# Performance work log

Measured on AMD Instinct MI355X. Metric: run time of the kernel, lower is better.

## Reference

```python
import jax, jax.numpy as jnp
import numpy as np

N_NODES = 50000


def _degree_norm(src, dst, n):
    # symmetric GCN normalization with self-loops already appended
    deg = jax.ops.segment_sum(jnp.ones(src.shape[0], jnp.float32), dst, num_segments=n)
    dinv = jnp.where(deg > 0, jax.lax.rsqrt(deg), 0.0)
    return dinv[src] * dinv[dst]  # [E_full]


def _gcn_layer(x, W, b, src, dst, norm, n):
    h = x @ W                                  # [N, out]
    msgs = h[src] * norm[:, None]              # gather + scale, [E_full, out]
    out = jax.ops.segment_sum(msgs, dst, num_segments=n)
    return out + b


def setup_inputs() -> dict:
    key = jax.random.key(0)
    k1, k2, k3, k4 = jax.random.split(key, 4)
    n, e, d_in, d_out = N_NODES, 800000, 256, 128
    x = jax.random.normal(k1, (n, d_in), jnp.float32)
    edge_index = jax.random.randint(k2, (2, e), 0, n, dtype=jnp.int64)
    W1 = jax.random.normal(k3, (d_in, 2 * d_out), jnp.float32) / np.sqrt(d_in)
    b1 = jnp.zeros((2 * d_out,), jnp.float32)
    W2 = jax.random.normal(k4, (2 * d_out, d_out), jnp.float32) / np.sqrt(2 * d_out)
    b2 = jnp.zeros((d_out,), jnp.float32)
    return {"x": x, "edge_index": edge_index, "W1": W1, "b1": b1, "W2": W2, "b2": b2}


def reference(x, edge_index, W1, b1, W2, b2):
    n = x.shape[0]
    loops = jnp.arange(n, dtype=edge_index.dtype)
    src = jnp.concatenate([edge_index[0], loops])
    dst = jnp.concatenate([edge_index[1], loops])
    norm = _degree_norm(src, dst, n)
    h = jax.nn.relu(_gcn_layer(x, W1, b1, src, dst, norm, n))
    h = jax.nn.relu(_gcn_layer(h, W2, b2, src, dst, norm, n))
    return h
```

## Files before the change

### kernel.cpp

```cpp
#include <hip/hip_runtime.h>
#include <hip/hip_bf16.h>


typedef __attribute__((ext_vector_type(8))) short bf16x8;
typedef __attribute__((ext_vector_type(8))) unsigned short u16x8;
typedef __attribute__((ext_vector_type(4))) float f32x4;

__device__ inline float bf2f(unsigned short u) {
    return __uint_as_float(((unsigned)u) << 16);
}
__device__ inline unsigned short f2bf(float f) {
    unsigned x = __float_as_uint(f);
    unsigned r = (x + 0x7fffu + ((x >> 16) & 1u)) >> 16;
    return (unsigned short)r;
}

__global__ void degree_kernel(const int* __restrict__ dst, unsigned* __restrict__ deg, int E) {
    int e = blockIdx.x * blockDim.x + threadIdx.x;
    if (e < E) atomicAdd(&deg[dst[e]], 1u);
}

__global__ void dinv_kernel(const unsigned* __restrict__ deg, float* __restrict__ dinv, int N) {
    int i = blockIdx.x * blockDim.x + threadIdx.x;
    if (i < N) dinv[i] = rsqrtf((float)(deg[i] + 1u));
}

#define NBIN 512

__global__ __launch_bounds__(256) void hist_lds_kernel(const unsigned* __restrict__ deg,
                                                       int* __restrict__ hist, int N) {
    __shared__ int lh[NBIN];
    const int t = threadIdx.x;
#pragma unroll
    for (int i = 0; i < NBIN / 256; i++) lh[t + i * 256] = 0;
    __syncthreads();
    int idx = blockIdx.x * 256 + t;
    if (idx < N) {
        int b = (int)deg[idx]; if (b > NBIN - 1) b = NBIN - 1;
        atomicAdd(&lh[NBIN - 1 - b], 1);
    }
    __syncthreads();
#pragma unroll
    for (int i = 0; i < NBIN / 256; i++) {
        int v = lh[t + i * 256];
        if (v) atomicAdd(&hist[t + i * 256], v);
    }
}

__global__ __launch_bounds__(256) void place_lds_kernel(const unsigned* __restrict__ deg,
                                                        int* __restrict__ hist,
                                                        int* __restrict__ perm, int N) {
    __shared__ int lh[NBIN];
    __shared__ int base[NBIN];
    const int t = threadIdx.x;
#pragma unroll
    for (int i = 0; i < NBIN / 256; i++) lh[t + i * 256] = 0;
    __syncthreads();
    int idx = blockIdx.x * 256 + t;
    int bin = 0, rank = 0;
    if (idx < N) {
        int b = (int)deg[idx]; if (b > NBIN - 1) b = NBIN - 1;
        bin = NBIN - 1 - b;
        rank = atomicAdd(&lh[bin], 1);
    }
    __syncthreads();
#pragma unroll
    for (int i = 0; i < NBIN / 256; i++) {
        int v = lh[t + i * 256];
        if (v) base[t + i * 256] = atomicAdd(&hist[t + i * 256], v);
    }
    __syncthreads();
    if (idx < N) perm[base[bin] + rank] = idx;
}

__global__ __launch_bounds__(256) void rank_kernel(const int* __restrict__ perm,
                                                   int* __restrict__ rank, int N) {
    int i = blockIdx.x * blockDim.x + threadIdx.x;
    if (i < N) rank[perm[i]] = i;
}

#define SCAN_CHUNK 2048

__global__ __launch_bounds__(256) void scan_phase1(const unsigned* __restrict__ deg,
                                                   const int* __restrict__ perm,
                                                   int* __restrict__ bsum, int N) {
    __shared__ int ws[4];
    const int t = threadIdx.x, lane = t & 63, w = t >> 6;
    int base = blockIdx.x * SCAN_CHUNK;
    int s = 0;
#pragma unroll
    for (int r = 0; r < SCAN_CHUNK / 256; r++) {
        int i = base + r * 256 + t;
        s += (i < N) ? (int)deg[perm[i]] : 0;
    }
#pragma unroll
    for (int off = 1; off < 64; off <<= 1) s += __shfl_xor(s, off, 64);
    if (lane == 0) ws[w] = s;
    __syncthreads();
    if (t == 0) bsum[blockIdx.x] = ws[0] + ws[1] + ws[2] + ws[3];
}

__global__ void scan_phase2(int* __restrict__ bsum, int nb) {
    const int t = threadIdx.x;
    int carry = 0;
    for (int b = 0; b < nb; b += 64) {
        int i = b + t;
        int v = (i < nb) ? bsum[i] : 0;
        int x = v;
#pragma unroll
        for (int off = 1; off < 64; off <<= 1) {
            int y = __shfl_up(x, off, 64);
            if (t >= off) x += y;
        }
        if (i < nb) bsum[i] = carry + x - v;
        carry += __shfl(x, 63, 64);
    }
}

__global__ __launch_bounds__(256) void scan_phase3(const unsigned* __restrict__ deg,
                                                   const int* __restrict__ perm,
                                                   const int* __restrict__ bsum,
                                                   int* __restrict__ rowptr,
                                                   int* __restrict__ cursor, int N) {
    __shared__ int ws[4];
    const int t = threadIdx.x, lane = t & 63, w = t >> 6;
    int base = blockIdx.x * SCAN_CHUNK;
    int carry = bsum[blockIdx.x];
#pragma unroll
    for (int r = 0; r < SCAN_CHUNK / 256; r++) {
        int i = base + r * 256 + t;
        int v = (i < N) ? (int)deg[perm[i]] : 0;
        int x = v;
#pragma unroll
        for (int off = 1; off < 64; off <<= 1) {
            int y = __shfl_up(x, off, 64);
            if (lane >= off) x += y;
        }
        if (lane == 63) ws[w] = x;
        __syncthreads();
        int wo = 0;
        for (int j = 0; j < w; j++) wo += ws[j];
        int excl = x + wo - v;
        if (i < N) { rowptr[i] = carry + excl; cursor[i] = carry + excl; }
        int total = ws[0] + ws[1] + ws[2] + ws[3];
        __syncthreads();
        carry += total;
    }
    if (blockIdx.x == gridDim.x - 1 && t == 0) rowptr[N] = carry;
}

__global__ __launch_bounds__(256) void fill_kernel(const int* __restrict__ src,
                                                   const int* __restrict__ dst,
                                                   const int* __restrict__ rank,
                                                   int* __restrict__ cursor,
                                                   unsigned short* __restrict__ col, int E) {
    int e = blockIdx.x * blockDim.x + threadIdx.x;
    if (e < E) {
        int d = dst[e];
        int pos = atomicAdd(&cursor[rank[d]], 1);
        col[pos] = (unsigned short)src[e];
    }
}

__global__ __launch_bounds__(256) void convert_x_kernel(const float* __restrict__ in,
                                                        const float* __restrict__ dinv,
                                                        unsigned short* __restrict__ out,
                                                        long n4, int ld4) {
    long i = (long)blockIdx.x * blockDim.x + threadIdx.x;
    if (i < n4) {
        float ds = dinv[i / ld4];
        float4 v = ((const float4*)in)[i];
        ushort4 o;
        o.x = f2bf(v.x * ds); o.y = f2bf(v.y * ds);
        o.z = f2bf(v.z * ds); o.w = f2bf(v.w * ds);
        ((ushort4*)out)[i] = o;
    }
}

__global__ __launch_bounds__(256) void convert_wt_kernel(const float* __restrict__ W,
                                                         unsigned short* __restrict__ WT,
                                                         int K, int Nw) {
    int id = blockIdx.x * blockDim.x + threadIdx.x;
    if (id < K * Nw) {
        int k = id / Nw;
        int n = id % Nw;
        WT[(long)n * K + k] = f2bf(W[id]);
    }
}

#define GBM 128
#define GBN 128
#define GBK 64
template <int CH>
__global__ __launch_bounds__(256) void gemm_bf16(const unsigned short* __restrict__ A,
                                                 const unsigned short* __restrict__ BT,
                                                 unsigned short* __restrict__ C,
                                                 int M, int Nc, int K) {
    __shared__ __align__(16) unsigned short As[GBM * GBK];
    __shared__ __align__(16) unsigned short Bs[GBN * GBK];
    const int t = threadIdx.x;
    const int lane = t & 63;
    const int w = t >> 6;
    const int row0 = blockIdx.x * GBM;
    const int col0 = blockIdx.y * GBN;
    const int rb = (w >> 1) * 64;
    const int cb = (w & 1) * 64;

    f32x4 acc[4][4] = {};

    for (int kb = 0; kb < K; kb += GBK) {
#pragma unroll
        for (int i = 0; i < 4; i++) {
            int p = i * 256 + t;
            int row = p >> 3;
            int slot = p & 7;
            int chunk = slot ^ (row & 7);
            int grow = row0 + row;
            if (grow >= M) grow = M - 1;
            const unsigned short* src = A + (size_t)grow * K + kb + chunk * 8;
            __builtin_amdgcn_global_load_lds(
                (const __attribute__((address_space(1))) void*)src,
                (__attribute__((address_space(3))) void*)&As[p * 8], 16, 0, 0);
        }
#pragma unroll
        for (int i = 0; i < 4; i++) {
            int p = i * 256 + t;
            int row = p >> 3;
            int slot = p & 7;
            int chunk = slot ^ (row & 7);
            const unsigned short* src = BT + (size_t)(col0 + row) * K + kb + chunk * 8;
            __builtin_amdgcn_global_load_lds(
                (const __attribute__((address_space(1))) void*)src,
                (__attribute__((address_space(3))) void*)&Bs[p * 8], 16, 0, 0);
        }
        asm volatile("s_waitcnt vmcnt(0)" ::: "memory");
        __syncthreads();

#pragma unroll
        for (int ks = 0; ks < 2; ks++) {
            int kq = ks * 4 + (lane >> 4);
            int rsel = lane & 15;
            bf16x8 af[4], bfr[4];
#pragma unroll
            for (int mt = 0; mt < 4; mt++) {
                int m = rb + mt * 16 + rsel;
                int slot = kq ^ (m & 7);
                af[mt] = *(const bf16x8*)&As[m * GBK + slot * 8];
            }
#pragma unroll
            for (int nt = 0; nt < 4; nt++) {
                int n = cb + nt * 16 + rsel;
                int slot = kq ^ (n & 7);
                bfr[nt] = *(const bf16x8*)&Bs[n * GBK + slot * 8];
            }
#pragma unroll
            for (int mt = 0; mt < 4; mt++)
#pragma unroll
                for (int nt = 0; nt < 4; nt++)
                    acc[mt][nt] = __builtin_amdgcn_mfma_f32_16x16x32_bf16(
                        af[mt], bfr[nt], acc[mt][nt], 0, 0, 0);
        }
        __syncthreads();
    }

#pragma unroll
    for (int mt = 0; mt < 4; mt++) {
#pragma unroll
        for (int nt = 0; nt < 4; nt++) {
            int gcol = col0 + cb + nt * 16 + (lane & 15);
            int c = gcol / CH;
            int fo = gcol % CH;
            int grow0 = row0 + rb + mt * 16 + 4 * (lane >> 4);
#pragma unroll
            for (int r = 0; r < 4; r++) {
                int g = grow0 + r;
                if (g < M)
                    C[((size_t)c * M + g) * CH + fo] = f2bf(acc[mt][nt][r]);
            }
        }
    }
}

template <int CH, int NCH, bool OUT_BF16>
__global__ __launch_bounds__(256) void gather_cm_kernel(
    const unsigned short* __restrict__ h_cm,
    const int* __restrict__ rowptr,
    const unsigned short* __restrict__ col,
    const int* __restrict__ perm,
    const float* __restrict__ dinv,
    const float* __restrict__ bias,
    void* __restrict__ out,
    int Nn, int F) {
    constexpr int LF = CH / 8;
    constexpr int NS = 64 / LF;
    constexpr int NPB = NS * 4;
    const int chunk = blockIdx.x % NCH;
    const int g = blockIdx.x / NCH;
    const int w = threadIdx.x >> 6;
    const int lane = threadIdx.x & 63;
    const int fl = lane & (LF - 1);
    const int ns = lane / LF;
    const int idx = g * NPB + w * NS + ns;
    const bool valid = idx < Nn;
    const int cidx = valid ? idx : Nn - 1;
    const int node = perm[cidx];

    const unsigned short* hc = h_cm + (size_t)chunk * Nn * CH;
    const int beg = rowptr[cidx];
    const int end = valid ? rowptr[cidx + 1] : beg;
    const float ddst = dinv[node];
    const int fo = fl * 8;

    float a[8] = {};
    int e = beg;
    for (; e + 4 <= end; e += 4) {
        int s0 = col[e], s1 = col[e + 1], s2 = col[e + 2], s3 = col[e + 3];
        u16x8 u0 = *(const u16x8*)(hc + s0 * CH + fo);
        u16x8 u1 = *(const u16x8*)(hc + s1 * CH + fo);
        u16x8 u2 = *(const u16x8*)(hc + s2 * CH + fo);
        u16x8 u3 = *(const u16x8*)(hc + s3 * CH + fo);
#pragma unroll
        for (int j = 0; j < 8; j++) {
            a[j] += (bf2f(u0[j]) + bf2f(u1[j])) + (bf2f(u2[j]) + bf2f(u3[j]));
        }
    }
    for (; e < end; e++) {
        int s = col[e];
        u16x8 u = *(const u16x8*)(hc + s * CH + fo);
#pragma unroll
        for (int j = 0; j < 8; j++) a[j] += bf2f(u[j]);
    }

    if (valid) {
        u16x8 us = *(const u16x8*)(hc + node * CH + fo);
        const int f0g = chunk * CH + fo;
        f32x4 bv0 = *(const f32x4*)(bias + f0g);
        f32x4 bv1 = *(const f32x4*)(bias + f0g + 4);
        float v[8];
#pragma unroll
        for (int j = 0; j < 8; j++) {
            float b = (j < 4) ? bv0[j] : bv1[j - 4];
            v[j] = fmaxf(fmaf(a[j] + bf2f(us[j]), ddst, b), 0.f);
        }
        if (OUT_BF16) {
            u16x8 o;
#pragma unroll
            for (int j = 0; j < 8; j++) o[j] = f2bf(v[j] * ddst);
            *(u16x8*)((unsigned short*)out + (size_t)node * F + f0g) = o;
        } else {
            f32x4 o0, o1;
#pragma unroll
            for (int j = 0; j < 4; j++) { o0[j] = v[j]; o1[j] = v[j + 4]; }
            float* op = (float*)out + (size_t)node * F + f0g;
            *(f32x4*)op = o0;
            *(f32x4*)(op + 4) = o1;
        }
    }
}

extern "C" void kernel_launch(void* const* d_in, const int* in_sizes, int n_in,
                              void* d_out, int out_size, void* d_ws, size_t ws_size,
                              hipStream_t stream) {
    const float* x  = (const float*)d_in[0];
    const int* ei   = (const int*)d_in[1];
    const float* W1 = (const float*)d_in[2];
    const float* b1 = (const float*)d_in[3];
    const float* W2 = (const float*)d_in[4];
    const float* b2 = (const float*)d_in[5];

    const int DIN = 256;
    const int N = in_sizes[0] / DIN;
    const int E = in_sizes[1] / 2;
    const int H = in_sizes[3];
    const int DOUT = in_sizes[5];

    const int* src = ei;
    const int* dst = ei + E;

    char* ws = (char*)d_ws;
    unsigned* deg = (unsigned*)ws;                   ws += (size_t)N * 4;
    float* dinv   = (float*)ws;                      ws += (size_t)N * 4;
    int* rowptr   = (int*)ws;                        ws += (size_t)(N + 4) * 4;
    int* bsum     = (int*)ws;                        ws += 64 * 4;
    int* hist     = (int*)ws;                        ws += NBIN * 4;
    int* perm     = (int*)ws;                        ws += (size_t)N * 4;
    int* rankv    = (int*)ws;                        ws += (size_t)N * 4;
    int* cursor   = (int*)ws;                        ws += (size_t)N * 4;
    unsigned short* col = (unsigned short*)ws;       ws += (size_t)E * 2;
    unsigned short* xb  = (unsigned short*)ws;       ws += (size_t)N * DIN * 2;
    unsigned short* w1t = (unsigned short*)ws;       ws += (size_t)DIN * H * 2;
    unsigned short* w2t = (unsigned short*)ws;       ws += (size_t)H * DOUT * 2;
    unsigned short* h1b = (unsigned short*)ws;       ws += (size_t)N * H * 2;
    unsigned short* y1b = (unsigned short*)ws;       ws += (size_t)N * H * 2;
    unsigned short* h2b = xb;
    float* outp = (float*)d_out;

    hipMemsetAsync(deg, 0, (size_t)N * 4, stream);
    hipMemsetAsync(hist, 0, (size_t)NBIN * 4, stream);
    degree_kernel<<<(E + 255) / 256, 256, 0, stream>>>(dst, deg, E);
    dinv_kernel<<<(N + 255) / 256, 256, 0, stream>>>(deg, dinv, N);
    hist_lds_kernel<<<(N + 255) / 256, 256, 0, stream>>>(deg, hist, N);
    scan_phase2<<<1, 64, 0, stream>>>(hist, NBIN);
    place_lds_kernel<<<(N + 255) / 256, 256, 0, stream>>>(deg, hist, perm, N);
    rank_kernel<<<(N + 255) / 256, 256, 0, stream>>>(perm, rankv, N);
    {
        int nb = (N + SCAN_CHUNK - 1) / SCAN_CHUNK;
        scan_phase1<<<nb, 256, 0, stream>>>(deg, perm, bsum, N);
        scan_phase2<<<1, 64, 0, stream>>>(bsum, nb);
        scan_phase3<<<nb, 256, 0, stream>>>(deg, perm, bsum, rowptr, cursor, N);
    }
    fill_kernel<<<(E + 255) / 256, 256, 0, stream>>>(src, dst, rankv, cursor, col, E);

    {
        long n4 = (long)N * DIN / 4;
        convert_x_kernel<<<(int)((n4 + 255) / 256), 256, 0, stream>>>(x, dinv, xb, n4, DIN / 4);
        convert_wt_kernel<<<(DIN * H + 255) / 256, 256, 0, stream>>>(W1, w1t, DIN, H);
        convert_wt_kernel<<<(H * DOUT + 255) / 256, 256, 0, stream>>>(W2, w2t, H, DOUT);
    }

    {
        dim3 grid((N + GBM - 1) / GBM, H / GBN);
        gemm_bf16<32><<<grid, 256, 0, stream>>>(xb, w1t, h1b, N, H, DIN);
    }
    {
        constexpr int NPB1 = (64 / (32 / 8)) * 4;
        gather_cm_kernel<32, 8, true><<<8 * ((N + NPB1 - 1) / NPB1), 256, 0, stream>>>(
            h1b, rowptr, col, perm, dinv, b1, y1b, N, H);
    }

    {
        dim3 grid((N + GBM - 1) / GBM, DOUT / GBN);
        gemm_bf16<32><<<grid, 256, 0, stream>>>(y1b, w2t, h2b, N, DOUT, H);
    }
    {
        constexpr int NPB2 = (64 / (32 / 8)) * 4;
        gather_cm_kernel<32, 4, false><<<4 * ((N + NPB2 - 1) / NPB2), 256, 0, stream>>>(
            h2b, rowptr, col, perm, dinv, b2, outp, N, DOUT);
    }
}
```

Before: 356.7 us.

## Derive CSR row pointers from degree-bin offsets and unroll gather by eight

```diff
diff --git a/kernel.cpp b/kernel.cpp
--- a/kernel.cpp
+++ b/kernel.cpp
@@ -47,9 +47,41 @@
     }
 }
 
-__global__ __launch_bounds__(256) void place_lds_kernel(const unsigned* __restrict__ deg,
-                                                        int* __restrict__ hist,
-                                                        int* __restrict__ perm, int N) {
+__global__ void scan_bins_kernel(const int* __restrict__ hist,
+                                 int* __restrict__ binstart,
+                                 int* __restrict__ bincur,
+                                 int* __restrict__ edgebase,
+                                 int* __restrict__ rowptr, int N, int E) {
+    const int t = threadIdx.x;
+    int cn = 0, ce = 0;
+    for (int b = 0; b < NBIN; b += 64) {
+        int i = b + t;
+        int cnt = hist[i];
+        int d = NBIN - 1 - i;
+        int en = cnt * d;
+        int xn = cnt, xe = en;
+#pragma unroll
+        for (int off = 1; off < 64; off <<= 1) {
+            int yn = __shfl_up(xn, off, 64);
+            int ye = __shfl_up(xe, off, 64);
+            if (t >= off) { xn += yn; xe += ye; }
+        }
+        binstart[i] = cn + xn - cnt;
+        bincur[i]   = cn + xn - cnt;
+        edgebase[i] = ce + xe - en;
+        cn += __shfl(xn, 63, 64);
+        ce += __shfl(xe, 63, 64);
+    }
+    if (t == 0) rowptr[N] = E;
+}
+
+__global__ __launch_bounds__(256) void place_fused_kernel(
+    const unsigned* __restrict__ deg,
+    int* __restrict__ bincur,
+    const int* __restrict__ binstart,
+    const int* __restrict__ edgebase,
+    int* __restrict__ perm, int* __restrict__ rankv,
+    int* __restrict__ rowptr, int* __restrict__ cursor, int N) {
     __shared__ int lh[NBIN];
     __shared__ int base[NBIN];
     const int t = threadIdx.x;
@@ -57,96 +89,28 @@
     for (int i = 0; i < NBIN / 256; i++) lh[t + i * 256] = 0;
     __syncthreads();
     int idx = blockIdx.x * 256 + t;
-    int bin = 0, rank = 0;
+    int bin = 0, lrank = 0;
     if (idx < N) {
         int b = (int)deg[idx]; if (b > NBIN - 1) b = NBIN - 1;
         bin = NBIN - 1 - b;
-        rank = atomicAdd(&lh[bin], 1);
+        lrank = atomicAdd(&lh[bin], 1);
     }
     __syncthreads();
 #pragma unroll
     for (int i = 0; i < NBIN / 256; i++) {
         int v = lh[t + i * 256];
-        if (v) base[t + i * 256] = atomicAdd(&hist[t + i * 256], v);
+        if (v) base[t + i * 256] = atomicAdd(&bincur[t + i * 256], v);
     }
     __syncthreads();
-    if (idx < N) perm[base[bin] + rank] = idx;
-}
-
-__global__ __launch_bounds__(256) void rank_kernel(const int* __restrict__ perm,
-                                                   int* __restrict__ rank, int N) {
-    int i = blockIdx.x * blockDim.x + threadIdx.x;
-    if (i < N) rank[perm[i]] = i;
-}
-
-#define SCAN_CHUNK 2048
-
-__global__ __launch_bounds__(256) void scan_phase1(const unsigned* __restrict__ deg,
-                                                   const int* __restrict__ perm,
-                                                   int* __restrict__ bsum, int N) {
-    __shared__ int ws[4];
-    const int t = threadIdx.x, lane = t & 63, w = t >> 6;
-    int base = blockIdx.x * SCAN_CHUNK;
-    int s = 0;
-#pragma unroll
-    for (int r = 0; r < SCAN_CHUNK / 256; r++) {
-        int i = base + r * 256 + t;
-        s += (i < N) ? (int)deg[perm[i]] : 0;
-    }
-#pragma unroll
-    for (int off = 1; off < 64; off <<= 1) s += __shfl_xor(s, off, 64);
-    if (lane == 0) ws[w] = s;
-    __syncthreads();
-    if (t == 0) bsum[blockIdx.x] = ws[0] + ws[1] + ws[2] + ws[3];
-}
-
-__global__ void scan_phase2(int* __restrict__ bsum, int nb) {
-    const int t = threadIdx.x;
-    int carry = 0;
-    for (int b = 0; b < nb; b += 64) {
-        int i = b + t;
-        int v = (i < nb) ? bsum[i] : 0;
-        int x = v;
-#pragma unroll
-        for (int off = 1; off < 64; off <<= 1) {
-            int y = __shfl_up(x, off, 64);
-            if (t >= off) x += y;
-        }
-        if (i < nb) bsum[i] = carry + x - v;
-        carry += __shfl(x, 63, 64);
-    }
-}
-
-__global__ __launch_bounds__(256) void scan_phase3(const unsigned* __restrict__ deg,
-                                                   const int* __restrict__ perm,
-                                                   const int* __restrict__ bsum,
-                                                   int* __restrict__ rowptr,
-                                                   int* __restrict__ cursor, int N) {
-    __shared__ int ws[4];
-    const int t = threadIdx.x, lane = t & 63, w = t >> 6;
-    int base = blockIdx.x * SCAN_CHUNK;
-    int carry = bsum[blockIdx.x];
-#pragma unroll
-    for (int r = 0; r < SCAN_CHUNK / 256; r++) {
-        int i = base + r * 256 + t;
-        int v = (i < N) ? (int)deg[perm[i]] : 0;
-        int x = v;
-#pragma unroll
-        for (int off = 1; off < 64; off <<= 1) {
-            int y = __shfl_up(x, off, 64);
-            if (lane >= off) x += y;
-        }
-        if (lane == 63) ws[w] = x;
-        __syncthreads();
-        int wo = 0;
-        for (int j = 0; j < w; j++) wo += ws[j];
-        int excl = x + wo - v;
-        if (i < N) { rowptr[i] = carry + excl; cursor[i] = carry + excl; }
-        int total = ws[0] + ws[1] + ws[2] + ws[3];
-        __syncthreads();
-        carry += total;
-    }
-    if (blockIdx.x == gridDim.x - 1 && t == 0) rowptr[N] = carry;
+    if (idx < N) {
+        int pos = base[bin] + lrank;
+        int d = NBIN - 1 - bin;
+        int rp = edgebase[bin] + (pos - binstart[bin]) * d;
+        perm[pos] = idx;
+        rankv[idx] = pos;
+        rowptr[pos] = rp;
+        cursor[pos] = rp;
+    }
 }
 
 __global__ __launch_bounds__(256) void fill_kernel(const int* __restrict__ src,
@@ -311,8 +275,25 @@
     const float ddst = dinv[node];
     const int fo = fl * 8;
 
-    float a[8] = {};
+    float a0[8] = {}, a1[8] = {};
     int e = beg;
+    for (; e + 8 <= end; e += 8) {
+        int s0 = col[e],     s1 = col[e + 1], s2 = col[e + 2], s3 = col[e + 3];
+        int s4 = col[e + 4], s5 = col[e + 5], s6 = col[e + 6], s7 = col[e + 7];
+        u16x8 u0 = *(const u16x8*)(hc + s0 * CH + fo);
+        u16x8 u1 = *(const u16x8*)(hc + s1 * CH + fo);
+        u16x8 u2 = *(const u16x8*)(hc + s2 * CH + fo);
+        u16x8 u3 = *(const u16x8*)(hc + s3 * CH + fo);
+        u16x8 u4 = *(const u16x8*)(hc + s4 * CH + fo);
+        u16x8 u5 = *(const u16x8*)(hc + s5 * CH + fo);
+        u16x8 u6 = *(const u16x8*)(hc + s6 * CH + fo);
+        u16x8 u7 = *(const u16x8*)(hc + s7 * CH + fo);
+#pragma unroll
+        for (int j = 0; j < 8; j++) {
+            a0[j] += (bf2f(u0[j]) + bf2f(u1[j])) + (bf2f(u2[j]) + bf2f(u3[j]));
+            a1[j] += (bf2f(u4[j]) + bf2f(u5[j])) + (bf2f(u6[j]) + bf2f(u7[j]));
+        }
+    }
     for (; e + 4 <= end; e += 4) {
         int s0 = col[e], s1 = col[e + 1], s2 = col[e + 2], s3 = col[e + 3];
         u16x8 u0 = *(const u16x8*)(hc + s0 * CH + fo);
@@ -321,14 +302,14 @@
         u16x8 u3 = *(const u16x8*)(hc + s3 * CH + fo);
 #pragma unroll
         for (int j = 0; j < 8; j++) {
-            a[j] += (bf2f(u0[j]) + bf2f(u1[j])) + (bf2f(u2[j]) + bf2f(u3[j]));
+            a0[j] += (bf2f(u0[j]) + bf2f(u1[j])) + (bf2f(u2[j]) + bf2f(u3[j]));
         }
     }
     for (; e < end; e++) {
         int s = col[e];
         u16x8 u = *(const u16x8*)(hc + s * CH + fo);
 #pragma unroll
-        for (int j = 0; j < 8; j++) a[j] += bf2f(u[j]);
+        for (int j = 0; j < 8; j++) a1[j] += bf2f(u[j]);
     }
 
     if (valid) {
@@ -340,7 +321,8 @@
 #pragma unroll
         for (int j = 0; j < 8; j++) {
             float b = (j < 4) ? bv0[j] : bv1[j - 4];
-            v[j] = fmaxf(fmaf(a[j] + bf2f(us[j]), ddst, b), 0.f);
+            float s = (a0[j] + a1[j]) + bf2f(us[j]);
+            v[j] = fmaxf(fmaf(s, ddst, b), 0.f);
         }
         if (OUT_BF16) {
             u16x8 o;
@@ -381,8 +363,10 @@
     unsigned* deg = (unsigned*)ws;                   ws += (size_t)N * 4;
     float* dinv   = (float*)ws;                      ws += (size_t)N * 4;
     int* rowptr   = (int*)ws;                        ws += (size_t)(N + 4) * 4;
-    int* bsum     = (int*)ws;                        ws += 64 * 4;
     int* hist     = (int*)ws;                        ws += NBIN * 4;
+    int* binstart = (int*)ws;                        ws += NBIN * 4;
+    int* bincur   = (int*)ws;                        ws += NBIN * 4;
+    int* edgebase = (int*)ws;                        ws += NBIN * 4;
     int* perm     = (int*)ws;                        ws += (size_t)N * 4;
     int* rankv    = (int*)ws;                        ws += (size_t)N * 4;
     int* cursor   = (int*)ws;                        ws += (size_t)N * 4;
@@ -400,15 +384,9 @@
     degree_kernel<<<(E + 255) / 256, 256, 0, stream>>>(dst, deg, E);
     dinv_kernel<<<(N + 255) / 256, 256, 0, stream>>>(deg, dinv, N);
     hist_lds_kernel<<<(N + 255) / 256, 256, 0, stream>>>(deg, hist, N);
-    scan_phase2<<<1, 64, 0, stream>>>(hist, NBIN);
-    place_lds_kernel<<<(N + 255) / 256, 256, 0, stream>>>(deg, hist, perm, N);
-    rank_kernel<<<(N + 255) / 256, 256, 0, stream>>>(perm, rankv, N);
-    {
-        int nb = (N + SCAN_CHUNK - 1) / SCAN_CHUNK;
-        scan_phase1<<<nb, 256, 0, stream>>>(deg, perm, bsum, N);
-        scan_phase2<<<1, 64, 0, stream>>>(bsum, nb);
-        scan_phase3<<<nb, 256, 0, stream>>>(deg, perm, bsum, rowptr, cursor, N);
-    }
+    scan_bins_kernel<<<1, 64, 0, stream>>>(hist, binstart, bincur, edgebase, rowptr, N, E);
+    place_fused_kernel<<<(N + 255) / 256, 256, 0, stream>>>(
+        deg, bincur, binstart, edgebase, perm, rankv, rowptr, cursor, N);
     fill_kernel<<<(E + 255) / 256, 256, 0, stream>>>(src, dst, rankv, cursor, col, E);
 
     {
```

Result: faster. 333.1 us (-6.6%).
